# Kernel tuning notes

Hardware: AMD Instinct MI355X
Metric: run time of the kernel (lower is better)

Reference implementation:

```python
import jax, jax.numpy as jnp
import numpy as np

N_USERS = 8192
D = 128
E = 262144        # known edges (nonzero_idx rows)
K = 131072        # static pad size for data-dependent candidate extraction
COS_THR = 0.3
TAU = 0.2


def setup_inputs() -> dict:
    key = jax.random.key(0)
    k1, k2, k3, k4 = jax.random.split(key, 4)
    user_emb = jax.random.normal(k1, (N_USERS, D), dtype=jnp.float32)
    nonzero_idx = jax.random.randint(k2, (E, 2), 0, N_USERS)
    W = jax.random.normal(k3, (2, 2 * D), dtype=jnp.float32) * 0.05  # mlp_s weight [2, 2*latent]
    b = jnp.zeros((2,), dtype=jnp.float32)                            # mlp_s bias
    gumbel_noise = jax.random.gumbel(k4, (E + K, 2), dtype=jnp.float32)
    return {"user_emb": user_emb, "W": W, "b": b,
            "gumbel_noise": gumbel_noise, "nonzero_idx": nonzero_idx}


def reference(user_emb, W, b, gumbel_noise, nonzero_idx):
    n = user_emb.shape[0]
    # ---- get_candidate_pair ----
    norm = jnp.linalg.norm(user_emb, axis=1, keepdims=True)
    u = user_emb / jnp.maximum(norm, 1e-12)          # F.normalize(dim=1)
    cos = u @ u.T                                    # [n, n]
    diag = jnp.arange(n)
    cos = cos.at[diag, diag].set(-1.0)               # fill_diagonal_(-1)
    cos = cos.at[nonzero_idx[:, 0], nonzero_idx[:, 1]].set(-1.0)
    mask = cos > COS_THR
    # static-size nonzero; padded slots point at (0,0) where cos == -1,
    # so they behave as invalid candidates (weight 0 downstream).
    ci, cj = jnp.nonzero(mask, size=K, fill_value=0)
    cand_vals = cos[ci, cj]                          # padded entries = -1
    cand_idx = jnp.stack([ci, cj], axis=1)           # [K, 2]

    # ---- forward ----
    pair_idx = jnp.concatenate([nonzero_idx, cand_idx], axis=0)   # [E+K, 2]
    u_emb = user_emb[pair_idx[:, 0]]
    v_emb = user_emb[pair_idx[:, 1]]
    concat_emb = jnp.concatenate([u_emb, v_emb], axis=1)          # [E+K, 2D]
    logits = concat_emb @ W.T + b                                 # [E+K, 2]

    # hard gumbel-softmax (straight-through)
    y_soft = jax.nn.softmax((logits + gumbel_noise) / TAU, axis=-1)
    y_hard = jax.nn.one_hot(jnp.argmax(y_soft, axis=-1), 2, dtype=y_soft.dtype)
    gumbel_output = y_hard + y_soft - jax.lax.stop_gradient(y_soft)
    gumbel_retain = gumbel_output[:, 0]                           # [E+K]

    # ---- get_edge_weight ----
    cand_w = jnp.maximum(cand_vals, 0.0)                          # masked_fill(<0, 0)
    weights = jnp.concatenate([jnp.ones((E,), dtype=cand_w.dtype), cand_w])
    w = gumbel_retain * weights                                   # [E+K]
    gumbel_01 = w
    gumbel_retain_w = jnp.concatenate([w[:, None], w[:, None]], axis=0)  # [2(E+K), 1]
    return gumbel_01, gumbel_retain_w, pair_idx
```

## Files before the change

### kernel.cpp

```cpp
#include <hip/hip_runtime.h>
#include <hip/hip_bf16.h>
#include <math.h>

#define N_USERS 8192
#define DIMS    128
#define EDGES   262144
#define KCAND   131072
#define NTOT    (EDGES + KCAND)
#define LISTCAP 131072
#define CAPB    512
#define NTILES  2080
#define COS_THR 0.3f
#define EPS_SEL 6e-3f
#define LOGIT_MARGIN 2e-3f

typedef short bf16x8 __attribute__((ext_vector_type(8)));
typedef float f32x4  __attribute__((ext_vector_type(4)));


__global__ __launch_bounds__(256) void prep_k(const float* __restrict__ x,
                                              const float* __restrict__ W,
                                              const int* __restrict__ nz,
                                              float* __restrict__ un,
                                              unsigned short* __restrict__ u0,
                                              float4* __restrict__ P,
                                              unsigned* __restrict__ excl) {
  if (blockIdx.x < 256) {
#pragma clang fp contract(off)
    const int tid  = threadIdx.x;
    const int rloc = tid >> 3;
    const int j    = tid & 7;
    const int i    = blockIdx.x * 32 + rloc;
    const float* r = x + (size_t)i * DIMS;

    float vals[16];
    float a = 0.f;
#pragma unroll
    for (int b8 = 0; b8 < 16; ++b8) {
      float t = r[b8 * 8 + j];
      vals[b8] = t;
      a = a + t * t;
    }
    a = a + __shfl_xor(a, 1, 64);
    a = a + __shfl_xor(a, 2, 64);
    float s = a + __shfl_xor(a, 4, 64);
    float n = (float)sqrt((double)s);
    n = fmaxf(n, 1e-12f);

    unsigned short* slab = u0 + (size_t)(i >> 7) * 16384 + (i & 127) * 8;
    float p0 = 0.f, p1 = 0.f, p2 = 0.f, p3 = 0.f;
#pragma unroll
    for (int b8 = 0; b8 < 16; ++b8) {
      int k = b8 * 8 + j;
      float t = vals[b8];
      float v = t / n;
      un[(size_t)i * DIMS + k] = v;
      __hip_bfloat16 h = __float2bfloat16(v);
      slab[(size_t)b8 * 1024 + j] = *(unsigned short*)&h;
      p0 = fmaf(t, W[k], p0);
      p1 = fmaf(t, W[128 + k], p1);
      p2 = fmaf(t, W[256 + k], p2);
      p3 = fmaf(t, W[384 + k], p3);
    }
#pragma unroll
    for (int m = 1; m < 8; m <<= 1) {
      p0 += __shfl_xor(p0, m, 64);
      p1 += __shfl_xor(p1, m, 64);
      p2 += __shfl_xor(p2, m, 64);
      p3 += __shfl_xor(p3, m, 64);
    }
    if (j == 0) P[i] = make_float4(p0, p1, p2, p3);
  } else {
    int t = (blockIdx.x - 256) * 256 + threadIdx.x;
    if (t < EDGES) {
      uint2 e = ((const uint2*)nz)[t];
      atomicOr(&excl[(size_t)e.x * 256 + (e.y >> 5)], 1u << (e.y & 31));
    }
  }
}

__global__ __launch_bounds__(512) void mfma_pass(const unsigned short* __restrict__ u0,
                                                 const float* __restrict__ un,
                                                 const unsigned* __restrict__ excl,
                                                 uint2* __restrict__ list,
                                                 int* __restrict__ gcount,
                                                 int* __restrict__ row_cnt) {
  __shared__ uint2 svec[CAPB];
  __shared__ int lcnt, lbase;

  const int tid  = threadIdx.x;
  const int lane = tid & 63;
  const int wv   = tid >> 6;
  const int quad = lane >> 4;
  const int l15  = lane & 15;

  int rem = blockIdx.x, bi = 0;
  while (rem >= 64 - bi) { rem -= 64 - bi; ++bi; }
  const int bj = bi + rem;
  const int I0 = bi * 128, J0 = bj * 128;
  const int moff = (wv & 3) * 32, noff = (wv >> 2) * 64;

  if (tid == 0) lcnt = 0;
  __syncthreads();

  const unsigned short* __restrict__ Abase = u0 + (size_t)bi * 16384;
  const unsigned short* __restrict__ Bbase = u0 + (size_t)bj * 16384;

  bf16x8 af[4][2], bfr[4][4];
#pragma unroll
  for (int kc = 0; kc < 4; ++kc) {
    const int cq = kc * 4 + quad;
#pragma unroll
    for (int mt = 0; mt < 2; ++mt)
      af[kc][mt] = *(const bf16x8*)&Abase[(size_t)(cq * 128 + moff + mt * 16 + l15) * 8];
#pragma unroll
    for (int nt = 0; nt < 4; ++nt)
      bfr[kc][nt] = *(const bf16x8*)&Bbase[(size_t)(cq * 128 + noff + nt * 16 + l15) * 8];
  }

  f32x4 acc[2][4];
#pragma unroll
  for (int mt = 0; mt < 2; ++mt)
#pragma unroll
    for (int nt = 0; nt < 4; ++nt)
#pragma unroll
      for (int g = 0; g < 4; ++g) acc[mt][nt][g] = 0.f;

#pragma unroll
  for (int kc = 0; kc < 4; ++kc)
#pragma unroll
    for (int mt = 0; mt < 2; ++mt)
#pragma unroll
      for (int nt = 0; nt < 4; ++nt)
        acc[mt][nt] = __builtin_amdgcn_mfma_f32_16x16x32_bf16(
            af[kc][mt], bfr[kc][nt], acc[mt][nt], 0, 0, 0);

#pragma unroll
  for (int mt = 0; mt < 2; ++mt)
#pragma unroll
    for (int nt = 0; nt < 4; ++nt)
#pragma unroll
      for (int g = 0; g < 4; ++g) {
        float v = acc[mt][nt][g];
        if (v > COS_THR - EPS_SEL) {
          int i = I0 + moff + mt * 16 + quad * 4 + g;
          int j = J0 + noff + nt * 16 + l15;
          if (j > i) {
            float vv = v;
            bool pass = true;
            if (v <= COS_THR + EPS_SEL) {
              const float* a = un + (size_t)i * DIMS;
              const float* bb = un + (size_t)j * DIMS;
              float s2 = 0.f;
              for (int k = 0; k < DIMS; ++k) s2 = fmaf(a[k], bb[k], s2);
              pass = (s2 > COS_THR);
              vv = s2;
            }
            if (pass) {
              unsigned wij = excl[(size_t)i * 256 + (j >> 5)];
              unsigned wji = excl[(size_t)j * 256 + (i >> 5)];
              unsigned uvv = __float_as_uint(vv);
              if (!((wij >> (j & 31)) & 1u)) {
                int idx = atomicAdd(&lcnt, 1);
                if (idx < CAPB) {
                  svec[idx] = make_uint2(((unsigned)i << 13) | j, uvv);
                  atomicAdd(&row_cnt[i], 1);
                }
              }
              if (!((wji >> (i & 31)) & 1u)) {
                int idx = atomicAdd(&lcnt, 1);
                if (idx < CAPB) {
                  svec[idx] = make_uint2(((unsigned)j << 13) | i, uvv);
                  atomicAdd(&row_cnt[j], 1);
                }
              }
            }
          }
        }
      }

  __syncthreads();
  int n = min(lcnt, CAPB);
  if (tid == 0) lbase = atomicAdd(gcount, n);
  __syncthreads();
  int base = lbase;
  for (int t = tid; t < n; t += 512) {
    int o = base + t;
    if (o < LISTCAP) list[o] = svec[t];
  }
}

__global__ __launch_bounds__(256) void scan8k(const int* __restrict__ cnt,
                                              int* __restrict__ off) {
  __shared__ int sm[256];
  int t = threadIdx.x;
  int base = t * 32;
  int s = 0;
  for (int i = 0; i < 32; ++i) s += cnt[base + i];
  sm[t] = s;
  __syncthreads();
  int x = s;
  for (int d = 1; d < 256; d <<= 1) {
    int y = (t >= d) ? sm[t - d] : 0;
    __syncthreads();
    x += y;
    sm[t] = x;
    __syncthreads();
  }
  int run = x - s;
  for (int i = 0; i < 32; ++i) { off[base + i] = run; run += cnt[base + i]; }
  if (t == 255) off[N_USERS] = x;
}

__global__ __launch_bounds__(256) void scatter_k(const uint2* __restrict__ list,
                                                 const int* __restrict__ gcount,
                                                 const int* __restrict__ row_off,
                                                 int* __restrict__ row_pos,
                                                 int* __restrict__ cand_i,
                                                 int* __restrict__ cand_j,
                                                 float* __restrict__ cand_v) {
  int t = blockIdx.x * 256 + threadIdx.x;
  int n = min(*gcount, LISTCAP);
  if (t >= n) return;
  uint2 e = list[t];
  int i = e.x >> 13, j = e.x & 8191;
  int pos = row_off[i] + atomicAdd(&row_pos[i], 1);
  if (pos < KCAND) {
    cand_i[pos] = i;
    cand_j[pos] = j;
    cand_v[pos] = __uint_as_float(e.y);
  }
}

__global__ __launch_bounds__(256) void sortrow_k(const int* __restrict__ row_off,
                                                 const int* __restrict__ row_cnt,
                                                 int* __restrict__ cand_j,
                                                 float* __restrict__ cand_v) {
  int r = blockIdx.x * 256 + threadIdx.x;
  if (r >= N_USERS) return;
  int o = row_off[r], c = row_cnt[r];
  if (o + c > KCAND) c = max(0, KCAND - o);
  for (int a = 1; a < c; ++a) {
    int jv = cand_j[o + a];
    float vv = cand_v[o + a];
    int b = a - 1;
    while (b >= 0 && cand_j[o + b] > jv) {
      cand_j[o + b + 1] = cand_j[o + b];
      cand_v[o + b + 1] = cand_v[o + b];
      --b;
    }
    cand_j[o + b + 1] = jv;
    cand_v[o + b + 1] = vv;
  }
}

__global__ __launch_bounds__(256) void finalize_k(const float* __restrict__ ue,
                                                  const float* __restrict__ W,
                                                  const float* __restrict__ b,
                                                  const float* __restrict__ g,
                                                  const int* __restrict__ nz,
                                                  const int* __restrict__ cand_i,
                                                  const int* __restrict__ cand_j,
                                                  const float* __restrict__ cand_v,
                                                  const int* __restrict__ row_off,
                                                  const float4* __restrict__ P,
                                                  float* __restrict__ out) {
  int p = blockIdx.x * 256 + threadIdx.x;
  if (p >= NTOT) return;

  int i, j;
  float wgt;
  if (p < EDGES) {
    i = nz[2 * p];
    j = nz[2 * p + 1];
    wgt = 1.0f;
  } else {
    int q = p - EDGES;
    if (q >= row_off[N_USERS]) {
      out[p] = 0.0f;
      out[NTOT + p] = 0.0f;
      out[2 * NTOT + p] = 0.0f;
      out[3 * NTOT + 2 * p + 0] = 0.0f;
      out[3 * NTOT + 2 * p + 1] = 0.0f;
      return;
    }
    i = cand_i[q];
    j = cand_j[q];
    wgt = fmaxf(cand_v[q], 0.0f);
  }

  float4 Pi = P[i], Pj = P[j];
  float l0 = Pi.x + Pj.y + b[0];
  float l1 = Pi.z + Pj.w + b[1];
  float g0 = g[2 * p], g1 = g[2 * p + 1];
  float s0 = l0 + g0, s1 = l1 + g1;

  if (fabsf(s0 - s1) < LOGIT_MARGIN) {
    const float* ri = ue + (size_t)i * DIMS;
    const float* rj = ue + (size_t)j * DIMS;
    float e0 = 0.f, e1 = 0.f;
    for (int k = 0; k < DIMS; ++k) {
      e0 = fmaf(ri[k], W[k], e0);
      e1 = fmaf(ri[k], W[256 + k], e1);
    }
    for (int k = 0; k < DIMS; ++k) {
      e0 = fmaf(rj[k], W[128 + k], e0);
      e1 = fmaf(rj[k], W[384 + k], e1);
    }
    s0 = (e0 + b[0]) + g0;
    s1 = (e1 + b[1]) + g1;
  }

  float w = (s0 >= s1) ? wgt : 0.0f;

  out[p] = w;
  out[NTOT + p] = w;
  out[2 * NTOT + p] = w;
  out[3 * NTOT + 2 * p + 0] = (float)i;
  out[3 * NTOT + 2 * p + 1] = (float)j;
}

extern "C" void kernel_launch(void* const* d_in, const int* in_sizes, int n_in,
                              void* d_out, int out_size, void* d_ws, size_t ws_size,
                              hipStream_t stream) {
  (void)in_sizes; (void)n_in; (void)out_size; (void)ws_size;

  const float* user_emb = (const float*)d_in[0];
  const float* W        = (const float*)d_in[1];
  const float* b        = (const float*)d_in[2];
  const float* gnoise   = (const float*)d_in[3];
  const int*   nz       = (const int*)d_in[4];
  float* out = (float*)d_out;

  char* ws = (char*)d_ws;
  float*          un      = (float*)(ws + 0);
  unsigned short* u0      = (unsigned short*)(ws + (4u << 20));
  unsigned*       excl    = (unsigned*)(ws + (6u << 20));
  char*           zbase   = ws + (14u << 20);
  int*            gcount  = (int*)(zbase);
  int*            row_cnt = (int*)(zbase + 64);
  int*            row_pos = (int*)(zbase + 64 + 32768);
  int*            row_off = (int*)(ws + (14u << 20) + (96u << 10));
  uint2*          list    = (uint2*)(ws + (15u << 20));
  int*            cand_i  = (int*)(ws + (16u << 20));
  int*            cand_j  = (int*)(ws + (16u << 20) + (512u << 10));
  float*          cand_v  = (float*)(ws + (17u << 20));
  float4*         P       = (float4*)(ws + (17u << 20) + (512u << 10));

  hipMemsetAsync(excl, 0, (8u << 20) + (96u << 10), stream);

  prep_k<<<256 + EDGES / 256, 256, 0, stream>>>(user_emb, W, nz, un, u0, P, excl);
  mfma_pass<<<NTILES, 512, 0, stream>>>(u0, un, excl, list, gcount, row_cnt);
  scan8k<<<1, 256, 0, stream>>>(row_cnt, row_off);
  scatter_k<<<LISTCAP / 256, 256, 0, stream>>>(list, gcount, row_off, row_pos,
                                               cand_i, cand_j, cand_v);
  sortrow_k<<<N_USERS / 256, 256, 0, stream>>>(row_off, row_cnt, cand_j, cand_v);
  finalize_k<<<NTOT / 256, 256, 0, stream>>>(user_emb, W, b, gnoise, nz,
                                             cand_i, cand_j, cand_v, row_off,
                                             P, out);
}
```

Baseline: 155.8 us.

## Move exclusion check and fp32 recheck out of MFMA tile epilogue into separate kernel

The MFMA tile kernel now only emits raw above-threshold pairs (both orientations) into the list, without consulting the exclusion bitmap or recomputing borderline cosines in fp32. A new resolve kernel walks the list, checks exclusion bits, does the fp32 dot product for borderline values, marks dead entries, and builds the per-row histogram. The aim is to strip divergent, latency-heavy global loads out of the compute-bound tile epilogue. In exchange it adds a kernel launch and list traffic, and excluded pairs now take up list and shared-buffer capacity that could overflow the caps.

```diff
diff --git a/kernel.cpp b/kernel.cpp
--- a/kernel.cpp
+++ b/kernel.cpp
@@ -13,6 +13,7 @@
 #define COS_THR 0.3f
 #define EPS_SEL 6e-3f
 #define LOGIT_MARGIN 2e-3f
+#define DEADKEY 0xFFFFFFFFu
 
 typedef short bf16x8 __attribute__((ext_vector_type(8)));
 typedef float f32x4  __attribute__((ext_vector_type(4)));
@@ -80,11 +81,8 @@
 }
 
 __global__ __launch_bounds__(512) void mfma_pass(const unsigned short* __restrict__ u0,
-                                                 const float* __restrict__ un,
-                                                 const unsigned* __restrict__ excl,
                                                  uint2* __restrict__ list,
-                                                 int* __restrict__ gcount,
-                                                 int* __restrict__ row_cnt) {
+                                                 int* __restrict__ gcount) {
   __shared__ uint2 svec[CAPB];
   __shared__ int lcnt, lbase;
 
@@ -146,34 +144,12 @@
           int i = I0 + moff + mt * 16 + quad * 4 + g;
           int j = J0 + noff + nt * 16 + l15;
           if (j > i) {
-            float vv = v;
-            bool pass = true;
-            if (v <= COS_THR + EPS_SEL) {
-              const float* a = un + (size_t)i * DIMS;
-              const float* bb = un + (size_t)j * DIMS;
-              float s2 = 0.f;
-              for (int k = 0; k < DIMS; ++k) s2 = fmaf(a[k], bb[k], s2);
-              pass = (s2 > COS_THR);
-              vv = s2;
-            }
-            if (pass) {
-              unsigned wij = excl[(size_t)i * 256 + (j >> 5)];
-              unsigned wji = excl[(size_t)j * 256 + (i >> 5)];
-              unsigned uvv = __float_as_uint(vv);
-              if (!((wij >> (j & 31)) & 1u)) {
-                int idx = atomicAdd(&lcnt, 1);
-                if (idx < CAPB) {
-                  svec[idx] = make_uint2(((unsigned)i << 13) | j, uvv);
-                  atomicAdd(&row_cnt[i], 1);
-                }
-              }
-              if (!((wji >> (i & 31)) & 1u)) {
-                int idx = atomicAdd(&lcnt, 1);
-                if (idx < CAPB) {
-                  svec[idx] = make_uint2(((unsigned)j << 13) | i, uvv);
-                  atomicAdd(&row_cnt[j], 1);
-                }
-              }
+            int idx = atomicAdd(&lcnt, 2);
+            if (idx + 1 < CAPB) {
+              svec[idx]     = make_uint2(((unsigned)i << 13) | j,
+                                         __float_as_uint(v));
+              svec[idx + 1] = make_uint2(((unsigned)j << 13) | i,
+                                         __float_as_uint(v));
             }
           }
         }
@@ -188,6 +164,31 @@
     int o = base + t;
     if (o < LISTCAP) list[o] = svec[t];
   }
+}
+
+__global__ __launch_bounds__(256) void resolve_hist_k(const float* __restrict__ un,
+                                                      const unsigned* __restrict__ excl,
+                                                      uint2* __restrict__ list,
+                                                      const int* __restrict__ gcount,
+                                                      int* __restrict__ row_cnt) {
+  int t = blockIdx.x * 256 + threadIdx.x;
+  int n = min(*gcount, LISTCAP);
+  if (t >= n) return;
+  uint2 e = list[t];
+  int i = e.x >> 13, j = e.x & 8191;
+  unsigned word = excl[(size_t)i * 256 + (j >> 5)];
+  bool alive = !((word >> (j & 31)) & 1u);
+  float v = __uint_as_float(e.y);
+  if (alive && v <= COS_THR + EPS_SEL) {
+    const float* a = un + (size_t)i * DIMS;
+    const float* b = un + (size_t)j * DIMS;
+    float s = 0.f;
+    for (int k = 0; k < DIMS; ++k) s = fmaf(a[k], b[k], s);
+    alive = (s > COS_THR);
+    if (alive) list[t] = make_uint2(e.x, __float_as_uint(s));
+  }
+  if (!alive) list[t] = make_uint2(DEADKEY, 0u);
+  else        atomicAdd(&row_cnt[i], 1);
 }
 
 __global__ __launch_bounds__(256) void scan8k(const int* __restrict__ cnt,
@@ -223,6 +224,7 @@
   int n = min(*gcount, LISTCAP);
   if (t >= n) return;
   uint2 e = list[t];
+  if (e.x == DEADKEY) return;
   int i = e.x >> 13, j = e.x & 8191;
   int pos = row_off[i] + atomicAdd(&row_pos[i], 1);
   if (pos < KCAND) {
@@ -350,7 +352,9 @@
   hipMemsetAsync(excl, 0, (8u << 20) + (96u << 10), stream);
 
   prep_k<<<256 + EDGES / 256, 256, 0, stream>>>(user_emb, W, nz, un, u0, P, excl);
-  mfma_pass<<<NTILES, 512, 0, stream>>>(u0, un, excl, list, gcount, row_cnt);
+  mfma_pass<<<NTILES, 512, 0, stream>>>(u0, list, gcount);
+  resolve_hist_k<<<LISTCAP / 256, 256, 0, stream>>>(un, excl, list, gcount,
+                                                    row_cnt);
   scan8k<<<1, 256, 0, stream>>>(row_cnt, row_off);
   scatter_k<<<LISTCAP / 256, 256, 0, stream>>>(list, gcount, row_off, row_pos,
                                                cand_i, cand_j, cand_v);
```

Measured after the change: 150.5 us. -3.4%, faster.
